# Kernel optimization log

Measured on AMD Instinct MI355X. Metric: run time of the kernel, lower is better.

## Reference

```python
import jax, jax.numpy as jnp
import numpy as np

B, N, D = 2, 2048, 768
HEADS, DIM_HEAD = 12, 64
INNER = HEADS * DIM_HEAD  # 768
OUT_DIM = 768


def setup_inputs() -> dict:
    key = jax.random.key(0)
    k1, k2, k3, k4, k5 = jax.random.split(key, 5)
    s_in = 1.0 / np.sqrt(D)
    s_inner = 1.0 / np.sqrt(INNER)
    return {
        "x": jax.random.normal(k1, (B, N, D), dtype=jnp.float32),
        "w_qkv": jax.random.normal(k2, (D, 3 * INNER), dtype=jnp.float32) * s_in,
        "b_qkv": jax.random.normal(k3, (3 * INNER,), dtype=jnp.float32) * 0.01,
        "w_out": jax.random.normal(k4, (INNER, OUT_DIM), dtype=jnp.float32) * s_inner,
        "b_out": jax.random.normal(k5, (OUT_DIM,), dtype=jnp.float32) * 0.01,
    }


def reference(x, w_qkv, b_qkv, w_out, b_out):
    b, n, _ = x.shape
    scale = DIM_HEAD ** -0.5
    qkv = x @ w_qkv + b_qkv                      # [b, n, 3*inner]
    q, k, v = jnp.split(qkv, 3, axis=-1)
    # 'b n (h d) -> b h n d'
    reshape = lambda t: t.reshape(b, n, HEADS, DIM_HEAD).transpose(0, 2, 1, 3)
    q, k, v = reshape(q), reshape(k), reshape(v)
    dots = jnp.einsum("bhnd,bhmd->bhnm", q, k) * scale
    attn = jax.nn.softmax(dots, axis=-1)
    out = jnp.einsum("bhnm,bhmd->bhnd", attn, v)  # [b, h, n, d]
    out = out.transpose(0, 2, 1, 3).reshape(b, n, INNER)
    return out @ w_out + b_out
```

## Files before the change

kernel.cpp:

```cpp
#include <hip/hip_runtime.h>
#include <hip/hip_bf16.h>
#include <stdint.h>


typedef __attribute__((ext_vector_type(8))) short bf16x8;
typedef __attribute__((ext_vector_type(4))) float f32x4;
typedef __attribute__((address_space(3))) unsigned int lds_uint;
typedef __attribute__((address_space(1))) const unsigned int g_uint;

__device__ __forceinline__ short f2bf(float f) {
    union { float f; uint32_t u; } x; x.f = f;
    uint32_t r = (x.u + 0x7fffu + ((x.u >> 16) & 1u)) >> 16;
    return (short)r;
}
__device__ __forceinline__ float exp2fast(float x) {
#if __has_builtin(__builtin_amdgcn_exp2f)
    return __builtin_amdgcn_exp2f(x);
#else
    return __expf(x * 0.6931471805599453f);
#endif
}
__device__ __forceinline__ void gl_lds16(const void* g, void* l) {
    __builtin_amdgcn_global_load_lds((g_uint*)g, (lds_uint*)l, 16, 0, 0);
}
#define WAITCNT_VM(N) asm volatile("s_waitcnt vmcnt(" #N ")" ::: "memory")
#define BARRIER_FENCED() do { __builtin_amdgcn_s_barrier(); \
                              asm volatile("" ::: "memory"); } while (0)

__device__ __forceinline__ void tr_tile(const float* __restrict__ W,
                                        short* __restrict__ Wt, int K, int N,
                                        int n0, int k0, int t, short* S) {
    {
        int kl = t >> 2, ng = t & 3;
        const float* src = W + (size_t)(k0 + kl) * N + n0 + ng * 16;
        #pragma unroll
        for (int j = 0; j < 16; j += 4) {
            float4 f = *(const float4*)(src + j);
            S[(ng*16 + j + 0) * 65 + kl] = f2bf(f.x);
            S[(ng*16 + j + 1) * 65 + kl] = f2bf(f.y);
            S[(ng*16 + j + 2) * 65 + kl] = f2bf(f.z);
            S[(ng*16 + j + 3) * 65 + kl] = f2bf(f.w);
        }
    }
    __syncthreads();
    {
        int nl = t >> 2, kg = t & 3;
        short* dst = Wt + (size_t)(n0 + nl) * K + k0 + kg * 16;
        #pragma unroll
        for (int j = 0; j < 16; j += 4) {
            short4 s4;
            s4.x = S[nl*65 + kg*16 + j + 0];
            s4.y = S[nl*65 + kg*16 + j + 1];
            s4.z = S[nl*65 + kg*16 + j + 2];
            s4.w = S[nl*65 + kg*16 + j + 3];
            *(short4*)(dst + j) = s4;
        }
    }
}

__global__ __launch_bounds__(256)
void prep_k(const float* __restrict__ x, short* __restrict__ Xb,
            const float* __restrict__ Wq, short* __restrict__ Wqt,
            const float* __restrict__ Wo, short* __restrict__ Wot)
{
    __shared__ short S[64 * 65];
    const int t = threadIdx.x;
    if (blockIdx.x < 1536) {
        int i = (blockIdx.x * 256 + t) * 8;
        float4 f0 = *(const float4*)(x + i);
        float4 f1 = *(const float4*)(x + i + 4);
        short s[8];
        s[0]=f2bf(f0.x); s[1]=f2bf(f0.y); s[2]=f2bf(f0.z); s[3]=f2bf(f0.w);
        s[4]=f2bf(f1.x); s[5]=f2bf(f1.y); s[6]=f2bf(f1.z); s[7]=f2bf(f1.w);
        *(uint4*)(Xb + i) = *(uint4*)s;
        return;
    }
    if (blockIdx.x < 1968) {
        const int b2 = blockIdx.x - 1536;
        tr_tile(Wq, Wqt, 768, 2304, (b2 % 36) * 64, (b2 / 36) * 64, t, S);
    } else {
        const int b3 = blockIdx.x - 1968;
        tr_tile(Wo, Wot, 768, 768, (b3 % 12) * 64, (b3 / 12) * 64, t, S);
    }
}

__global__ __launch_bounds__(256)
void tr_w(const float* __restrict__ W, short* __restrict__ Wt, int K, int N) {
    __shared__ short S[64 * 65];
    tr_tile(W, Wt, K, N, blockIdx.x * 64, blockIdx.y * 64, threadIdx.x, S);
}

__global__ __launch_bounds__(256)
void gemm_qkv(const short* __restrict__ A, const short* __restrict__ Bt,
              const float* __restrict__ bias,
              short* __restrict__ Qb, short* __restrict__ Kb, short* __restrict__ Vt)
{
    __shared__ short As[3][128 * 32];
    __shared__ short Bs[3][96 * 32];
    const int tid = threadIdx.x, lane = tid & 63, w = tid >> 6;
    const int wm = w >> 1, wn = w & 1, quad = lane >> 4, lcol = lane & 15;

    const int id = blockIdx.x;
    const int xcd = id & 7, j = id >> 3;
    const int bm = (xcd * 4 + (j / 24)) * 128;
    const int bn = (j % 24) * 96;

    f32x4 acc[4][3];
    #pragma unroll
    for (int i = 0; i < 4; i++)
        #pragma unroll
        for (int jj = 0; jj < 3; jj++) acc[i][jj] = (f32x4){0.f, 0.f, 0.f, 0.f};

    const int ar0 = tid >> 2,         ac0 = (tid & 3) * 8;
    const int ar1 = (tid + 256) >> 2;
    const int c2  = 256 + tid;
    const int br1 = c2 >> 2,          bc1 = (c2 & 3) * 8;

    const short* pA0 = A  + (size_t)(bm + ar0) * 768 + ac0;
    const short* pA1 = A  + (size_t)(bm + ar1) * 768 + ac0;
    const short* pB0 = Bt + (size_t)(bn + ar0) * 768 + ac0;
    const short* pB1 = Bt + (size_t)(bn + br1) * 768 + bc1;

    #pragma unroll
    for (int t0 = 0; t0 < 2; t0++) {
        const int kt = t0 * 32;
        gl_lds16(pA0 + kt, As[t0] + tid * 8);
        gl_lds16(pA1 + kt, As[t0] + (tid + 256) * 8);
        gl_lds16(pB0 + kt, Bs[t0] + tid * 8);
        if (tid < 128)
            gl_lds16(pB1 + kt, Bs[t0] + c2 * 8);
    }
    if (w < 2) { WAITCNT_VM(4); } else { WAITCNT_VM(3); }
    BARRIER_FENCED();

    #pragma unroll
    for (int it = 0; it < 24; it++) {
        const int p = it % 3;
        if (it < 22) {
            const int pb = (it + 2) % 3, kt = (it + 2) * 32;
            gl_lds16(pA0 + kt, As[pb] + tid * 8);
            gl_lds16(pA1 + kt, As[pb] + (tid + 256) * 8);
            gl_lds16(pB0 + kt, Bs[pb] + tid * 8);
            if (tid < 128)
                gl_lds16(pB1 + kt, Bs[pb] + c2 * 8);
        }
        bf16x8 a[4], b[3];
        #pragma unroll
        for (int tm = 0; tm < 4; tm++)
            a[tm] = *(const bf16x8*)(As[p] + (wm*64 + tm*16 + lcol) * 32 + quad * 8);
        #pragma unroll
        for (int tn = 0; tn < 3; tn++)
            b[tn] = *(const bf16x8*)(Bs[p] + (wn*48 + tn*16 + lcol) * 32 + quad * 8);
        #pragma unroll
        for (int tm = 0; tm < 4; tm++)
            #pragma unroll
            for (int tn = 0; tn < 3; tn++)
                acc[tm][tn] = __builtin_amdgcn_mfma_f32_16x16x32_bf16(a[tm], b[tn], acc[tm][tn], 0, 0, 0);
        if (it < 23) {
            if (it < 22) {
                if (w < 2) { WAITCNT_VM(4); } else { WAITCNT_VM(3); }
            } else {
                WAITCNT_VM(0);
            }
            BARRIER_FENCED();
        }
    }

    const float SCLQ = 0.18033688011112042f;
    #pragma unroll
    for (int tm = 0; tm < 4; tm++) {
        #pragma unroll
        for (int tn = 0; tn < 3; tn++) {
            int col = bn + wn*48 + tn*16 + lcol;
            float bv = bias[col];
            int which = (col >= 1536) ? 2 : (col >= 768 ? 1 : 0);
            int cc = col - which * 768;
            int h = cc >> 6, d = cc & 63;
            int rowbase = bm + wm*64 + tm*16 + quad*4;
            int bb = rowbase >> 11, n0 = rowbase & 2047;
            int bh = bb * 12 + h;
            if (which == 2) {
                short4 s4;
                s4.x = f2bf(acc[tm][tn][0] + bv);
                s4.y = f2bf(acc[tm][tn][1] + bv);
                s4.z = f2bf(acc[tm][tn][2] + bv);
                s4.w = f2bf(acc[tm][tn][3] + bv);
                *(short4*)(Vt + (((size_t)bh*32 + (n0 >> 6))*64 + d)*64 + (n0 & 63)) = s4;
            } else {
                #pragma unroll
                for (int reg = 0; reg < 4; reg++) {
                    float v = acc[tm][tn][reg] + bv;
                    if (which == 0) v *= SCLQ;
                    short* dst = (which == 0) ? Qb : Kb;
                    dst[((size_t)bh*2048 + n0 + reg)*64 + d] = f2bf(v);
                }
            }
        }
    }
}

#define ATTN_STEP(P, PB, DO_PRE, WMODE) do {                                   \
    if (DO_PRE) {                                                              \
        gl_lds16(pK0, Ks[PB] + c0 * 8);                                        \
        gl_lds16(pV0, Vs[PB] + c0 * 8);                                        \
        gl_lds16(pK1, Ks[PB] + c1 * 8);                                        \
        gl_lds16(pV1, Vs[PB] + c1 * 8);                                        \
        pK0 += 4096; pV0 += 4096; pK1 += 4096; pV1 += 4096;                    \
    }                                                                          \
    f32x4 st[4];                                                               \
    _Pragma("unroll")                                                          \
    for (int kvs = 0; kvs < 4; kvs++) st[kvs] = (f32x4){0.f, 0.f, 0.f, 0.f};   \
    _Pragma("unroll")                                                          \
    for (int ks = 0; ks < 2; ks++) {                                           \
        _Pragma("unroll")                                                      \
        for (int kvs = 0; kvs < 4; kvs++) {                                    \
            bf16x8 kf = *(const bf16x8*)(Ks[P] + (kvs*16 + lcol) * 64 +        \
                                         (((ks*4 + quad) ^ ksw) << 3));        \
            st[kvs] = __builtin_amdgcn_mfma_f32_16x16x32_bf16(kf, qf[ks],      \
                                                              st[kvs], 0, 0, 0); \
        }                                                                      \
    }                                                                          \
    uint32_t X[4], Y[4];                                                       \
    _Pragma("unroll")                                                          \
    for (int kvs = 0; kvs < 4; kvs++) {                                        \
        float p0 = exp2fast(st[kvs][0]), p1 = exp2fast(st[kvs][1]);            \
        float p2 = exp2fast(st[kvs][2]), p3 = exp2fast(st[kvs][3]);            \
        lp += (p0 + p1) + (p2 + p3);                                           \
        asm("v_cvt_pk_bf16_f32 %0, %1, %2" : "=v"(X[kvs]) : "v"(p0), "v"(p1)); \
        asm("v_cvt_pk_bf16_f32 %0, %1, %2" : "=v"(Y[kvs]) : "v"(p2), "v"(p3)); \
    }                                                                          \
    bf16x8 pa[2];                                                              \
    _Pragma("unroll")                                                          \
    for (int ks = 0; ks < 2; ks++) {                                           \
        uint32_t a0 = X[2*ks], a1 = X[2*ks + 1];                               \
        uint32_t b0 = Y[2*ks], b1 = Y[2*ks + 1];                               \
        asm("v_permlane16_swap_b32 %0, %1" : "+v"(a0), "+v"(a1));              \
        asm("v_permlane16_swap_b32 %0, %1" : "+v"(b0), "+v"(b1));              \
        union { uint32_t u[4]; bf16x8 v; } pk_;                                \
        pk_.u[0] = a0; pk_.u[1] = b0; pk_.u[2] = a1; pk_.u[3] = b1;            \
        pa[ks] = pk_.v;                                                        \
    }                                                                          \
    _Pragma("unroll")                                                          \
    for (int ks = 0; ks < 2; ks++) {                                           \
        _Pragma("unroll")                                                      \
        for (int tn = 0; tn < 4; tn++) {                                       \
            int row = tn * 16 + lcol;                                          \
            bf16x8 bv = *(const bf16x8*)(Vs[P] + row * 64 +                    \
                                         (((ks*4 + bq) ^ (row & 7)) << 3));    \
            o[tn] = __builtin_amdgcn_mfma_f32_16x16x32_bf16(pa[ks], bv,        \
                                                            o[tn], 0, 0, 0);   \
        }                                                                      \
    }                                                                          \
    if (WMODE == 0) { WAITCNT_VM(4); BARRIER_FENCED(); }                       \
    else if (WMODE == 1) { WAITCNT_VM(0); BARRIER_FENCED(); }                  \
} while (0)

__global__ __launch_bounds__(256)
void attn_k(const short* __restrict__ Q, const short* __restrict__ K,
            const short* __restrict__ Vt, short* __restrict__ Ab)
{
    __shared__ __align__(16) short Ks[3][4096];
    __shared__ __align__(16) short Vs[3][4096];

    const int tid = threadIdx.x, lane = tid & 63, w = tid >> 6;
    const int quad = lane >> 4, lcol = lane & 15;
    const int bid = blockIdx.x;
    const int bh = bid % 24, qt = bid / 24;
    const int b = bh / 12, h = bh - b * 12;

    const short* Kg = K  + (size_t)bh * 131072;
    const short* Vg = Vt + (size_t)bh * 131072;

    bf16x8 qf[2];
    {
        const short* Qg = Q + ((size_t)bh * 2048 + (size_t)qt * 64) * 64;
        #pragma unroll
        for (int ks = 0; ks < 2; ks++)
            qf[ks] = *(const bf16x8*)(Qg + (w*16 + lcol) * 64 + ks*32 + quad*8);
    }

    const int c0 = tid, c1 = tid + 256;
    const int r0 = c0 >> 3, s0 = r0 * 64 + (((c0 & 7) ^ (r0 & 7)) << 3);
    const int r1 = c1 >> 3, s1 = r1 * 64 + (((c1 & 7) ^ (r1 & 7)) << 3);

    #pragma unroll
    for (int t0 = 0; t0 < 2; t0++) {
        gl_lds16(Kg + t0 * 4096 + s0, Ks[t0] + c0 * 8);
        gl_lds16(Vg + t0 * 4096 + s0, Vs[t0] + c0 * 8);
        gl_lds16(Kg + t0 * 4096 + s1, Ks[t0] + c1 * 8);
        gl_lds16(Vg + t0 * 4096 + s1, Vs[t0] + c1 * 8);
    }
    WAITCNT_VM(4);
    BARRIER_FENCED();

    const short* pK0 = Kg + 2 * 4096 + s0;
    const short* pV0 = Vg + 2 * 4096 + s0;
    const short* pK1 = Kg + 2 * 4096 + s1;
    const short* pV1 = Vg + 2 * 4096 + s1;

    f32x4 o[4];
    #pragma unroll
    for (int tn = 0; tn < 4; tn++) o[tn] = (f32x4){0.f, 0.f, 0.f, 0.f};
    float lp = 0.f;

    const int ksw = lcol & 7;
    const int bq  = ((quad & 1) << 1) | (quad >> 1);

    for (int g = 0; g < 10; g++) {
        ATTN_STEP(0, 2, true, 0);
        ATTN_STEP(1, 0, true, 0);
        ATTN_STEP(2, 1, true, 0);
    }
    ATTN_STEP(0, 0, false, 1);
    ATTN_STEP(1, 0, false, 2);

    lp += __shfl_xor(lp, 16, 64);
    lp += __shfl_xor(lp, 32, 64);
    float rl[4];
    #pragma unroll
    for (int r = 0; r < 4; r++)
        rl[r] = 1.0f / __shfl(lp, quad * 4 + r, 64);

    #pragma unroll
    for (int tn = 0; tn < 4; tn++) {
        #pragma unroll
        for (int r = 0; r < 4; r++) {
            int q = qt * 64 + w * 16 + quad * 4 + r;
            int d = h * 64 + tn * 16 + lcol;
            Ab[((size_t)(b * 2048 + q)) * 768 + d] = f2bf(o[tn][r] * rl[r]);
        }
    }
}

__global__ __launch_bounds__(256)
void gemm_out(const short* __restrict__ A, const short* __restrict__ Bt,
              const float* __restrict__ bias, float* __restrict__ Of)
{
    __shared__ short As[3][64 * 32];
    __shared__ short Bs[3][96 * 32];
    const int tid = threadIdx.x, lane = tid & 63, w = tid >> 6;
    const int wm = w >> 1, wn = w & 1, quad = lane >> 4, lcol = lane & 15;

    const int id = blockIdx.x;
    const int xcd = id & 7, j = id >> 3;
    const int bm = (xcd * 8 + (j >> 3)) * 64;
    const int bn = (j & 7) * 96;

    f32x4 acc[2][3];
    #pragma unroll
    for (int i = 0; i < 2; i++)
        #pragma unroll
        for (int jj = 0; jj < 3; jj++) acc[i][jj] = (f32x4){0.f, 0.f, 0.f, 0.f};

    const int ar0 = tid >> 2, ac0 = (tid & 3) * 8;
    const int c2  = 256 + tid;
    const int br1 = c2 >> 2,  bc1 = (c2 & 3) * 8;

    const short* pA0 = A  + (size_t)(bm + ar0) * 768 + ac0;
    const short* pB0 = Bt + (size_t)(bn + ar0) * 768 + ac0;
    const short* pB1 = Bt + (size_t)(bn + br1) * 768 + bc1;

    #pragma unroll
    for (int t0 = 0; t0 < 2; t0++) {
        const int kt = t0 * 32;
        gl_lds16(pA0 + kt, As[t0] + tid * 8);
        gl_lds16(pB0 + kt, Bs[t0] + tid * 8);
        if (tid < 128)
            gl_lds16(pB1 + kt, Bs[t0] + c2 * 8);
    }
    if (w < 2) { WAITCNT_VM(3); } else { WAITCNT_VM(2); }
    BARRIER_FENCED();

    #pragma unroll
    for (int it = 0; it < 24; it++) {
        const int p = it % 3;
        if (it < 22) {
            const int pb = (it + 2) % 3, kt = (it + 2) * 32;
            gl_lds16(pA0 + kt, As[pb] + tid * 8);
            gl_lds16(pB0 + kt, Bs[pb] + tid * 8);
            if (tid < 128)
                gl_lds16(pB1 + kt, Bs[pb] + c2 * 8);
        }
        bf16x8 a[2], b[3];
        #pragma unroll
        for (int tm = 0; tm < 2; tm++)
            a[tm] = *(const bf16x8*)(As[p] + (wm*32 + tm*16 + lcol) * 32 + quad * 8);
        #pragma unroll
        for (int tn = 0; tn < 3; tn++)
            b[tn] = *(const bf16x8*)(Bs[p] + (wn*48 + tn*16 + lcol) * 32 + quad * 8);
        #pragma unroll
        for (int tm = 0; tm < 2; tm++)
            #pragma unroll
            for (int tn = 0; tn < 3; tn++)
                acc[tm][tn] = __builtin_amdgcn_mfma_f32_16x16x32_bf16(a[tm], b[tn], acc[tm][tn], 0, 0, 0);
        if (it < 23) {
            if (it < 22) {
                if (w < 2) { WAITCNT_VM(3); } else { WAITCNT_VM(2); }
            } else {
                WAITCNT_VM(0);
            }
            BARRIER_FENCED();
        }
    }
    #pragma unroll
    for (int tm = 0; tm < 2; tm++) {
        #pragma unroll
        for (int tn = 0; tn < 3; tn++) {
            int col = bn + wn*48 + tn*16 + lcol;
            float bv = bias[col];
            #pragma unroll
            for (int reg = 0; reg < 4; reg++) {
                int row = bm + wm*32 + tm*16 + quad*4 + reg;
                Of[(size_t)row * 768 + col] = acc[tm][tn][reg] + bv;
            }
        }
    }
}

extern "C" void kernel_launch(void* const* d_in, const int* in_sizes, int n_in,
                              void* d_out, int out_size, void* d_ws, size_t ws_size,
                              hipStream_t stream)
{
    (void)in_sizes; (void)n_in; (void)out_size;
    const float* x     = (const float*)d_in[0];
    const float* w_qkv = (const float*)d_in[1];
    const float* b_qkv = (const float*)d_in[2];
    const float* w_out = (const float*)d_in[3];
    const float* b_out = (const float*)d_in[4];
    float* out = (float*)d_out;

    const size_t XSZ = (size_t)4096 * 768;
    const size_t WQ  = (size_t)2304 * 768;
    const size_t WO  = (size_t)768 * 768;
    const size_t HSZ = (size_t)24 * 2048 * 64;
    short* Xb  = (short*)d_ws;
    short* Wqt = Xb + XSZ;
    short* Qb  = Wqt + WQ;
    short* Kb  = Qb + HSZ;
    short* Vt  = Kb + HSZ;
    short* Ab  = Xb;

    const bool sepWot = ws_size >= (XSZ + WQ + 3*HSZ + WO) * sizeof(short);
    short* Wot = sepWot ? (Vt + HSZ) : Wqt;

    if (sepWot) {
        prep_k<<<2112, 256, 0, stream>>>(x, Xb, w_qkv, Wqt, w_out, Wot);
        gemm_qkv<<<768, 256, 0, stream>>>(Xb, Wqt, b_qkv, Qb, Kb, Vt);
    } else {
        prep_k<<<1968, 256, 0, stream>>>(x, Xb, w_qkv, Wqt, w_out, Wot);
        gemm_qkv<<<768, 256, 0, stream>>>(Xb, Wqt, b_qkv, Qb, Kb, Vt);
        tr_w<<<dim3(12, 12), 256, 0, stream>>>(w_out, Wot, 768, 768);
    }
    attn_k<<<768, 256, 0, stream>>>(Qb, Kb, Vt, Ab);
    gemm_out<<<512, 256, 0, stream>>>(Ab, Wot, b_out, out);
}
```

Measured before the change: 152.3 us.

## Load GEMM A operand directly from global into registers, bypassing LDS

In both the QKV and output-projection GEMMs, the A tile is no longer staged through shared memory. Each wave loads its own A fragments straight from global memory into a two-deep register buffer, while B keeps the three-stage LDS pipeline with adjusted vmcnt waits. This removes A's LDS writes and reads and frees LDS, but raises register pressure and issues less coalesced per-lane 16-byte global loads. A rows are also re-read by both wn waves.

Measured after the change: 171.5 us. 1.13x slower.

```diff
diff --git a/kernel.cpp b/kernel.cpp
--- a/kernel.cpp
+++ b/kernel.cpp
@@ -95,7 +95,6 @@
               const float* __restrict__ bias,
               short* __restrict__ Qb, short* __restrict__ Kb, short* __restrict__ Vt)
 {
-    __shared__ short As[3][128 * 32];
     __shared__ short Bs[3][96 * 32];
     const int tid = threadIdx.x, lane = tid & 63, w = tid >> 6;
     const int wm = w >> 1, wn = w & 1, quad = lane >> 4, lcol = lane & 15;
@@ -111,54 +110,56 @@
         #pragma unroll
         for (int jj = 0; jj < 3; jj++) acc[i][jj] = (f32x4){0.f, 0.f, 0.f, 0.f};
 
-    const int ar0 = tid >> 2,         ac0 = (tid & 3) * 8;
-    const int ar1 = (tid + 256) >> 2;
+    const int ar0 = tid >> 2,  ac0 = (tid & 3) * 8;
     const int c2  = 256 + tid;
-    const int br1 = c2 >> 2,          bc1 = (c2 & 3) * 8;
-
-    const short* pA0 = A  + (size_t)(bm + ar0) * 768 + ac0;
-    const short* pA1 = A  + (size_t)(bm + ar1) * 768 + ac0;
+    const int br1 = c2 >> 2,   bc1 = (c2 & 3) * 8;
+
     const short* pB0 = Bt + (size_t)(bn + ar0) * 768 + ac0;
     const short* pB1 = Bt + (size_t)(bn + br1) * 768 + bc1;
 
+    const short* pA[4];
+    #pragma unroll
+    for (int tm = 0; tm < 4; tm++)
+        pA[tm] = A + (size_t)(bm + wm*64 + tm*16 + lcol) * 768 + quad * 8;
+
+    bf16x8 areg[2][4];
     #pragma unroll
     for (int t0 = 0; t0 < 2; t0++) {
         const int kt = t0 * 32;
-        gl_lds16(pA0 + kt, As[t0] + tid * 8);
-        gl_lds16(pA1 + kt, As[t0] + (tid + 256) * 8);
         gl_lds16(pB0 + kt, Bs[t0] + tid * 8);
         if (tid < 128)
             gl_lds16(pB1 + kt, Bs[t0] + c2 * 8);
-    }
-    if (w < 2) { WAITCNT_VM(4); } else { WAITCNT_VM(3); }
+        #pragma unroll
+        for (int tm = 0; tm < 4; tm++)
+            areg[t0][tm] = *(const bf16x8*)(pA[tm] + kt);
+    }
+    if (w < 2) { WAITCNT_VM(6); } else { WAITCNT_VM(5); }
     BARRIER_FENCED();
 
     #pragma unroll
     for (int it = 0; it < 24; it++) {
-        const int p = it % 3;
+        const int p = it % 3, s = it & 1;
+        bf16x8 b[3];
+        #pragma unroll
+        for (int tn = 0; tn < 3; tn++)
+            b[tn] = *(const bf16x8*)(Bs[p] + (wn*48 + tn*16 + lcol) * 32 + quad * 8);
+        #pragma unroll
+        for (int tm = 0; tm < 4; tm++)
+            #pragma unroll
+            for (int tn = 0; tn < 3; tn++)
+                acc[tm][tn] = __builtin_amdgcn_mfma_f32_16x16x32_bf16(areg[s][tm], b[tn], acc[tm][tn], 0, 0, 0);
         if (it < 22) {
             const int pb = (it + 2) % 3, kt = (it + 2) * 32;
-            gl_lds16(pA0 + kt, As[pb] + tid * 8);
-            gl_lds16(pA1 + kt, As[pb] + (tid + 256) * 8);
             gl_lds16(pB0 + kt, Bs[pb] + tid * 8);
             if (tid < 128)
                 gl_lds16(pB1 + kt, Bs[pb] + c2 * 8);
-        }
-        bf16x8 a[4], b[3];
-        #pragma unroll
-        for (int tm = 0; tm < 4; tm++)
-            a[tm] = *(const bf16x8*)(As[p] + (wm*64 + tm*16 + lcol) * 32 + quad * 8);
-        #pragma unroll
-        for (int tn = 0; tn < 3; tn++)
-            b[tn] = *(const bf16x8*)(Bs[p] + (wn*48 + tn*16 + lcol) * 32 + quad * 8);
-        #pragma unroll
-        for (int tm = 0; tm < 4; tm++)
             #pragma unroll
-            for (int tn = 0; tn < 3; tn++)
-                acc[tm][tn] = __builtin_amdgcn_mfma_f32_16x16x32_bf16(a[tm], b[tn], acc[tm][tn], 0, 0, 0);
+            for (int tm = 0; tm < 4; tm++)
+                areg[s][tm] = *(const bf16x8*)(pA[tm] + kt);
+        }
         if (it < 23) {
             if (it < 22) {
-                if (w < 2) { WAITCNT_VM(4); } else { WAITCNT_VM(3); }
+                if (w < 2) { WAITCNT_VM(10); } else { WAITCNT_VM(9); }
             } else {
                 WAITCNT_VM(0);
             }
@@ -336,7 +337,6 @@
 void gemm_out(const short* __restrict__ A, const short* __restrict__ Bt,
               const float* __restrict__ bias, float* __restrict__ Of)
 {
-    __shared__ short As[3][64 * 32];
     __shared__ short Bs[3][96 * 32];
     const int tid = threadIdx.x, lane = tid & 63, w = tid >> 6;
     const int wm = w >> 1, wn = w & 1, quad = lane >> 4, lcol = lane & 15;
@@ -356,46 +356,52 @@
     const int c2  = 256 + tid;
     const int br1 = c2 >> 2,  bc1 = (c2 & 3) * 8;
 
-    const short* pA0 = A  + (size_t)(bm + ar0) * 768 + ac0;
     const short* pB0 = Bt + (size_t)(bn + ar0) * 768 + ac0;
     const short* pB1 = Bt + (size_t)(bn + br1) * 768 + bc1;
 
+    const short* pA[2];
+    #pragma unroll
+    for (int tm = 0; tm < 2; tm++)
+        pA[tm] = A + (size_t)(bm + wm*32 + tm*16 + lcol) * 768 + quad * 8;
+
+    bf16x8 areg[2][2];
     #pragma unroll
     for (int t0 = 0; t0 < 2; t0++) {
         const int kt = t0 * 32;
-        gl_lds16(pA0 + kt, As[t0] + tid * 8);
         gl_lds16(pB0 + kt, Bs[t0] + tid * 8);
         if (tid < 128)
             gl_lds16(pB1 + kt, Bs[t0] + c2 * 8);
-    }
-    if (w < 2) { WAITCNT_VM(3); } else { WAITCNT_VM(2); }
+        #pragma unroll
+        for (int tm = 0; tm < 2; tm++)
+            areg[t0][tm] = *(const bf16x8*)(pA[tm] + kt);
+    }
+    if (w < 2) { WAITCNT_VM(4); } else { WAITCNT_VM(3); }
     BARRIER_FENCED();
 
     #pragma unroll
     for (int it = 0; it < 24; it++) {
-        const int p = it % 3;
+        const int p = it % 3, s = it & 1;
+        bf16x8 b[3];
+        #pragma unroll
+        for (int tn = 0; tn < 3; tn++)
+            b[tn] = *(const bf16x8*)(Bs[p] + (wn*48 + tn*16 + lcol) * 32 + quad * 8);
+        #pragma unroll
+        for (int tm = 0; tm < 2; tm++)
+            #pragma unroll
+            for (int tn = 0; tn < 3; tn++)
+                acc[tm][tn] = __builtin_amdgcn_mfma_f32_16x16x32_bf16(areg[s][tm], b[tn], acc[tm][tn], 0, 0, 0);
         if (it < 22) {
             const int pb = (it + 2) % 3, kt = (it + 2) * 32;
-            gl_lds16(pA0 + kt, As[pb] + tid * 8);
             gl_lds16(pB0 + kt, Bs[pb] + tid * 8);
             if (tid < 128)
                 gl_lds16(pB1 + kt, Bs[pb] + c2 * 8);
-        }
-        bf16x8 a[2], b[3];
-        #pragma unroll
-        for (int tm = 0; tm < 2; tm++)
-            a[tm] = *(const bf16x8*)(As[p] + (wm*32 + tm*16 + lcol) * 32 + quad * 8);
-        #pragma unroll
-        for (int tn = 0; tn < 3; tn++)
-            b[tn] = *(const bf16x8*)(Bs[p] + (wn*48 + tn*16 + lcol) * 32 + quad * 8);
-        #pragma unroll
-        for (int tm = 0; tm < 2; tm++)
             #pragma unroll
-            for (int tn = 0; tn < 3; tn++)
-                acc[tm][tn] = __builtin_amdgcn_mfma_f32_16x16x32_bf16(a[tm], b[tn], acc[tm][tn], 0, 0, 0);
+            for (int tm = 0; tm < 2; tm++)
+                areg[s][tm] = *(const bf16x8*)(pA[tm] + kt);
+        }
         if (it < 23) {
             if (it < 22) {
-                if (w < 2) { WAITCNT_VM(3); } else { WAITCNT_VM(2); }
+                if (w < 2) { WAITCNT_VM(6); } else { WAITCNT_VM(5); }
             } else {
                 WAITCNT_VM(0);
             }
```

## Halve QKV GEMM M-tile to 64 rows and switch to double buffering

Applied to the files above, without the earlier changes.

The QKV projection GEMM now uses 64x96 tiles instead of 128x96, doubling the grid to 1536 blocks so the CUs get more waves and a more even tail. The 3-stage LDS pipeline with per-wave vmcnt waits is replaced by a simpler 2-stage double buffer that uses __syncthreads after every K step. The intent is better occupancy and load balance. In exchange there is less data reuse per block, more global traffic for the B matrix, and a shallower prefetch, so load latency is less well hidden.

New measurement: 163.7 us. 7.5% more time.

```diff
diff --git a/kernel.cpp b/kernel.cpp
--- a/kernel.cpp
+++ b/kernel.cpp
@@ -95,80 +95,64 @@
               const float* __restrict__ bias,
               short* __restrict__ Qb, short* __restrict__ Kb, short* __restrict__ Vt)
 {
-    __shared__ short As[3][128 * 32];
-    __shared__ short Bs[3][96 * 32];
+    __shared__ short As[2][64 * 32];
+    __shared__ short Bs[2][96 * 32];
     const int tid = threadIdx.x, lane = tid & 63, w = tid >> 6;
     const int wm = w >> 1, wn = w & 1, quad = lane >> 4, lcol = lane & 15;
 
     const int id = blockIdx.x;
     const int xcd = id & 7, j = id >> 3;
-    const int bm = (xcd * 4 + (j / 24)) * 128;
+    const int bm = (xcd * 8 + (j / 24)) * 64;
     const int bn = (j % 24) * 96;
 
-    f32x4 acc[4][3];
-    #pragma unroll
-    for (int i = 0; i < 4; i++)
+    f32x4 acc[2][3];
+    #pragma unroll
+    for (int i = 0; i < 2; i++)
         #pragma unroll
         for (int jj = 0; jj < 3; jj++) acc[i][jj] = (f32x4){0.f, 0.f, 0.f, 0.f};
 
-    const int ar0 = tid >> 2,         ac0 = (tid & 3) * 8;
-    const int ar1 = (tid + 256) >> 2;
+    const int ar0 = tid >> 2, ac0 = (tid & 3) * 8;
     const int c2  = 256 + tid;
-    const int br1 = c2 >> 2,          bc1 = (c2 & 3) * 8;
+    const int br1 = c2 >> 2,  bc1 = (c2 & 3) * 8;
 
     const short* pA0 = A  + (size_t)(bm + ar0) * 768 + ac0;
-    const short* pA1 = A  + (size_t)(bm + ar1) * 768 + ac0;
     const short* pB0 = Bt + (size_t)(bn + ar0) * 768 + ac0;
     const short* pB1 = Bt + (size_t)(bn + br1) * 768 + bc1;
 
-    #pragma unroll
-    for (int t0 = 0; t0 < 2; t0++) {
-        const int kt = t0 * 32;
-        gl_lds16(pA0 + kt, As[t0] + tid * 8);
-        gl_lds16(pA1 + kt, As[t0] + (tid + 256) * 8);
-        gl_lds16(pB0 + kt, Bs[t0] + tid * 8);
-        if (tid < 128)
-            gl_lds16(pB1 + kt, Bs[t0] + c2 * 8);
-    }
-    if (w < 2) { WAITCNT_VM(4); } else { WAITCNT_VM(3); }
-    BARRIER_FENCED();
+    gl_lds16(pA0, As[0] + tid * 8);
+    gl_lds16(pB0, Bs[0] + tid * 8);
+    if (tid < 128)
+        gl_lds16(pB1, Bs[0] + c2 * 8);
+    __syncthreads();
 
     #pragma unroll
     for (int it = 0; it < 24; it++) {
-        const int p = it % 3;
-        if (it < 22) {
-            const int pb = (it + 2) % 3, kt = (it + 2) * 32;
-            gl_lds16(pA0 + kt, As[pb] + tid * 8);
-            gl_lds16(pA1 + kt, As[pb] + (tid + 256) * 8);
-            gl_lds16(pB0 + kt, Bs[pb] + tid * 8);
+        const int p = it & 1;
+        if (it < 23) {
+            const int kt = (it + 1) * 32;
+            gl_lds16(pA0 + kt, As[p ^ 1] + tid * 8);
+            gl_lds16(pB0 + kt, Bs[p ^ 1] + tid * 8);
             if (tid < 128)
-                gl_lds16(pB1 + kt, Bs[pb] + c2 * 8);
-        }
-        bf16x8 a[4], b[3];
-        #pragma unroll
-        for (int tm = 0; tm < 4; tm++)
-            a[tm] = *(const bf16x8*)(As[p] + (wm*64 + tm*16 + lcol) * 32 + quad * 8);
+                gl_lds16(pB1 + kt, Bs[p ^ 1] + c2 * 8);
+        }
+        bf16x8 a[2], b[3];
+        #pragma unroll
+        for (int tm = 0; tm < 2; tm++)
+            a[tm] = *(const bf16x8*)(As[p] + (wm*32 + tm*16 + lcol) * 32 + quad * 8);
         #pragma unroll
         for (int tn = 0; tn < 3; tn++)
             b[tn] = *(const bf16x8*)(Bs[p] + (wn*48 + tn*16 + lcol) * 32 + quad * 8);
         #pragma unroll
-        for (int tm = 0; tm < 4; tm++)
+        for (int tm = 0; tm < 2; tm++)
             #pragma unroll
             for (int tn = 0; tn < 3; tn++)
                 acc[tm][tn] = __builtin_amdgcn_mfma_f32_16x16x32_bf16(a[tm], b[tn], acc[tm][tn], 0, 0, 0);
-        if (it < 23) {
-            if (it < 22) {
-                if (w < 2) { WAITCNT_VM(4); } else { WAITCNT_VM(3); }
-            } else {
-                WAITCNT_VM(0);
-            }
-            BARRIER_FENCED();
-        }
+        __syncthreads();
     }
 
     const float SCLQ = 0.18033688011112042f;
     #pragma unroll
-    for (int tm = 0; tm < 4; tm++) {
+    for (int tm = 0; tm < 2; tm++) {
         #pragma unroll
         for (int tn = 0; tn < 3; tn++) {
             int col = bn + wn*48 + tn*16 + lcol;
@@ -176,7 +160,7 @@
             int which = (col >= 1536) ? 2 : (col >= 768 ? 1 : 0);
             int cc = col - which * 768;
             int h = cc >> 6, d = cc & 63;
-            int rowbase = bm + wm*64 + tm*16 + quad*4;
+            int rowbase = bm + wm*32 + tm*16 + quad*4;
             int bb = rowbase >> 11, n0 = rowbase & 2047;
             int bh = bb * 12 + h;
             if (which == 2) {
@@ -445,10 +429,10 @@
 
     if (sepWot) {
         prep_k<<<2112, 256, 0, stream>>>(x, Xb, w_qkv, Wqt, w_out, Wot);
-        gemm_qkv<<<768, 256, 0, stream>>>(Xb, Wqt, b_qkv, Qb, Kb, Vt);
+        gemm_qkv<<<1536, 256, 0, stream>>>(Xb, Wqt, b_qkv, Qb, Kb, Vt);
     } else {
         prep_k<<<1968, 256, 0, stream>>>(x, Xb, w_qkv, Wqt, w_out, Wot);
-        gemm_qkv<<<768, 256, 0, stream>>>(Xb, Wqt, b_qkv, Qb, Kb, Vt);
+        gemm_qkv<<<1536, 256, 0, stream>>>(Xb, Wqt, b_qkv, Qb, Kb, Vt);
         tr_w<<<dim3(12, 12), 256, 0, stream>>>(w_out, Wot, 768, 768);
     }
     attn_k<<<768, 256, 0, stream>>>(Qb, Kb, Vt, Ab);
```
